# Performance work log

Hardware: AMD Instinct MI355X
Metric: run time of the kernel (lower is better)

Reference implementation:

```python
import jax, jax.numpy as jnp
import numpy as np

B, N, M, K = 128, 20000, 85400, 3  # trajectories, variables, clauses, literals/clause


def setup_inputs() -> dict:
    key = jax.random.key(0)
    k_v, k_idx, k_sign, k_xs = jax.random.split(key, 4)
    v = jax.random.normal(k_v, (B, N), dtype=jnp.float32)
    input_idx = jax.random.randint(k_idx, (B, M, K), 0, N, dtype=jnp.int32)
    # literal signs are exactly +/-1
    input_sign = jnp.where(jax.random.normal(k_sign, (B, M, K)) > 0, 1.0, -1.0).astype(jnp.float32)
    xl = jnp.ones((B, M), dtype=jnp.float32)            # long-term memory (init 1)
    xs = jax.random.uniform(k_xs, (B, M), dtype=jnp.float32)  # short-term memory in [0,1]
    # [alpha, beta, gamma, delta, epsilon, zeta] -- typical MemComputing coefficients
    param = jnp.array([5.0, 20.0, 0.25, 0.05, 0.001, 0.1], dtype=jnp.float32)
    return {"v": v, "xl": xl, "xs": xs, "param": param,
            "input_sign": input_sign, "input_idx": input_idx}


def reference(v, xl, xs, param, input_sign, input_idx):
    """Faithful port of OR.calc_grad. Returns (C, grad_v, dxl, dxs)."""
    b = v.shape[0]
    k = input_idx.shape[-1]
    alpha, beta, gamma, delta, epsilon, zeta = param
    b_idx = jnp.arange(b)[:, None, None]                # (B,1,1)
    inp = v[b_idx, input_idx] * input_sign              # (B,M,K) gather + sign
    v_top, v_top_idx = jax.lax.top_k(inp, 2)            # top-2 literal values per clause
    v_top = (1.0 - v_top) * 0.5                         # transform; v_top[...,0] is smallest -> C
    C = v_top[..., 0]                                   # (B,M) clause 'distance to satisfied'
    hot = jax.nn.one_hot(v_top_idx[..., 0], k, dtype=v.dtype)  # (B,M,K) mask of max literal
    # G: C everywhere, second-best value at the max-literal slot, scaled by xl*xs
    G = jnp.where(hot > 0, v_top[..., 1:2], C[..., None]) * (xl * xs)[..., None]
    # R: C only at the max-literal slot, scaled by (1+zeta*xl)*(1-xs)
    R = hot * C[..., None] * ((1.0 + zeta * xl) * (1.0 - xs))[..., None]
    dv = -(G + R) * input_sign                          # (B,M,K)
    grad_v = jnp.zeros_like(v).at[b_idx, input_idx].add(dv)  # scatter-add over dim 1
    dxl = -alpha * (C - delta)                          # (B,M)
    dxs = -beta * (xs + epsilon) * (C - gamma)          # (B,M)
    return C, grad_v, dxl, dxs
```

## Files before the change

### kernel.cpp

```cpp
#include <hip/hip_runtime.h>


#define NMAX 20000
#define BPB  4

typedef int   int4v   __attribute__((ext_vector_type(4)));
typedef float float4v __attribute__((ext_vector_type(4)));

__device__ __forceinline__ void clause_math(
    float a0, float a1, float a2, float xlv, float xsv, float zeta,
    float& C, float& g0, float& g1, float& g2)
{
    int k0; float m0, m1;
    if (a0 >= a1) {
        if (a0 >= a2) { k0 = 0; m0 = a0; m1 = fmaxf(a1, a2); }
        else          { k0 = 2; m0 = a2; m1 = fmaxf(a0, a1); }
    } else {
        if (a1 >= a2) { k0 = 1; m0 = a1; m1 = fmaxf(a0, a2); }
        else          { k0 = 2; m0 = a2; m1 = fmaxf(a0, a1); }
    }
    C = (1.f - m0) * 0.5f;
    const float T2 = (1.f - m1) * 0.5f;
    const float gl = xlv * xsv;
    const float rC = C * ((1.f + zeta * xlv) * (1.f - xsv));
    g0 = (k0 == 0 ? T2 : C) * gl + (k0 == 0 ? rC : 0.f);
    g1 = (k0 == 1 ? T2 : C) * gl + (k0 == 1 ? rC : 0.f);
    g2 = (k0 == 2 ? T2 : C) * gl + (k0 == 2 ? rC : 0.f);
}

__global__ __launch_bounds__(1024, 1) void or_priv2(
    const float* __restrict__ v,
    const float* __restrict__ xl,
    const float* __restrict__ xs,
    const float* __restrict__ param,
    const float* __restrict__ sign,
    const int*   __restrict__ idx,
    float* __restrict__ outC,
    float* __restrict__ outdxl,
    float* __restrict__ outdxs,
    float* __restrict__ partial,
    int N, int M, int chunk)
{
    __shared__ float sv[NMAX];
    __shared__ float sg[NMAX];
    const int j = blockIdx.x;
    const int b = blockIdx.y;
    const int tid = threadIdx.x;

    {
        const float4v* __restrict__ v4 = (const float4v*)(v + (size_t)b * N);
        float4v* sv4 = (float4v*)sv;
        float4v* sg4 = (float4v*)sg;
        const int n4 = N >> 2;
        const float4v z = {0.f, 0.f, 0.f, 0.f};
        for (int i = tid; i < n4; i += 1024) {
            sv4[i] = v4[i];
            sg4[i] = z;
        }
        for (int i = (n4 << 2) + tid; i < N; i += 1024) {
            sv[i] = v[(size_t)b * N + i];
            sg[i] = 0.f;
        }
    }
    __syncthreads();

    const float alpha = param[0], beta = param[1], gamma = param[2];
    const float delta = param[3], eps  = param[4], zeta  = param[5];

    const int mstart = j * chunk;
    const int mend   = min(M, mstart + chunk);
    const int ngroups = (mend > mstart) ? ((mend - mstart + 3) >> 2) : 0;

    for (int g = tid; g < ngroups; g += 1024) {
        const int m0 = mstart + (g << 2);
        const size_t base = (size_t)b * M + m0;

        if (m0 + 3 < mend) {
            const int4v*   __restrict__ ip = (const int4v*)(idx + base * 3);
            const float4v* __restrict__ sp = (const float4v*)(sign + base * 3);
            const int4v   ia = __builtin_nontemporal_load(ip + 0);
            const int4v   ib = __builtin_nontemporal_load(ip + 1);
            const int4v   ic = __builtin_nontemporal_load(ip + 2);
            const float4v sa = __builtin_nontemporal_load(sp + 0);
            const float4v sb = __builtin_nontemporal_load(sp + 1);
            const float4v sc = __builtin_nontemporal_load(sp + 2);
            const float4v xl4 = __builtin_nontemporal_load((const float4v*)(xl + base));
            const float4v xs4 = __builtin_nontemporal_load((const float4v*)(xs + base));

            const int   ii[12] = {ia.x, ia.y, ia.z, ia.w, ib.x, ib.y, ib.z, ib.w,
                                  ic.x, ic.y, ic.z, ic.w};
            const float ss[12] = {sa.x, sa.y, sa.z, sa.w, sb.x, sb.y, sb.z, sb.w,
                                  sc.x, sc.y, sc.z, sc.w};
            const float xlA[4] = {xl4.x, xl4.y, xl4.z, xl4.w};
            const float xsA[4] = {xs4.x, xs4.y, xs4.z, xs4.w};
            float Cv[4], dxlv[4], dxsv[4];

            #pragma unroll
            for (int c = 0; c < 4; ++c) {
                const int   i0 = ii[3*c], i1 = ii[3*c+1], i2 = ii[3*c+2];
                const float s0 = ss[3*c], s1 = ss[3*c+1], s2 = ss[3*c+2];
                const float a0 = sv[i0] * s0, a1 = sv[i1] * s1, a2 = sv[i2] * s2;
                float C, g0, g1, g2;
                clause_math(a0, a1, a2, xlA[c], xsA[c], zeta, C, g0, g1, g2);
                atomicAdd(&sg[i0], -g0 * s0);
                atomicAdd(&sg[i1], -g1 * s1);
                atomicAdd(&sg[i2], -g2 * s2);
                Cv[c]   = C;
                dxlv[c] = -alpha * (C - delta);
                dxsv[c] = -beta * (xsA[c] + eps) * (C - gamma);
            }
            const float4v cv  = {Cv[0], Cv[1], Cv[2], Cv[3]};
            const float4v lv  = {dxlv[0], dxlv[1], dxlv[2], dxlv[3]};
            const float4v svo = {dxsv[0], dxsv[1], dxsv[2], dxsv[3]};
            __builtin_nontemporal_store(cv,  (float4v*)(outC + base));
            __builtin_nontemporal_store(lv,  (float4v*)(outdxl + base));
            __builtin_nontemporal_store(svo, (float4v*)(outdxs + base));
        } else {
            for (int m = m0; m < mend; ++m) {
                const size_t bm  = (size_t)b * M + m;
                const size_t bm3 = bm * 3;
                const int   i0 = idx[bm3 + 0], i1 = idx[bm3 + 1], i2 = idx[bm3 + 2];
                const float s0 = sign[bm3 + 0], s1 = sign[bm3 + 1], s2 = sign[bm3 + 2];
                const float a0 = sv[i0] * s0, a1 = sv[i1] * s1, a2 = sv[i2] * s2;
                const float xlv = xl[bm], xsv = xs[bm];
                float C, g0, g1, g2;
                clause_math(a0, a1, a2, xlv, xsv, zeta, C, g0, g1, g2);
                atomicAdd(&sg[i0], -g0 * s0);
                atomicAdd(&sg[i1], -g1 * s1);
                atomicAdd(&sg[i2], -g2 * s2);
                outC[bm]   = C;
                outdxl[bm] = -alpha * (C - delta);
                outdxs[bm] = -beta * (xsv + eps) * (C - gamma);
            }
        }
    }
    __syncthreads();

    {
        float* __restrict__ pj = partial + ((size_t)j * gridDim.y + b) * N;
        const float4v* sg4 = (const float4v*)sg;
        const int n4 = N >> 2;
        for (int i = tid; i < n4; i += 1024)
            __builtin_nontemporal_store(sg4[i], (float4v*)pj + i);
        for (int i = (n4 << 2) + tid; i < N; i += 1024) pj[i] = sg[i];
    }
}

__global__ __launch_bounds__(256) void reduce4(
    const float4v* __restrict__ p, float4v* __restrict__ out, int n4, int stride4)
{
    int i = blockIdx.x * 256 + threadIdx.x;
    const int gs = gridDim.x * 256;
    for (; i < n4; i += gs) {
        const float4v a = p[i];
        const float4v b = p[i + stride4];
        const float4v c = p[i + 2 * stride4];
        const float4v d = p[i + 3 * stride4];
        out[i] = a + b + c + d;
    }
}

__global__ __launch_bounds__(256) void zero_f4(float4v* __restrict__ p, int n4) {
    int i = blockIdx.x * blockDim.x + threadIdx.x;
    int stride = gridDim.x * blockDim.x;
    const float4v z = {0.f, 0.f, 0.f, 0.f};
    for (; i < n4; i += stride) p[i] = z;
}

__global__ __launch_bounds__(256) void or_kernel(
    const float* __restrict__ v, const float* __restrict__ xl,
    const float* __restrict__ xs, const float* __restrict__ param,
    const float* __restrict__ sign, const int* __restrict__ idx,
    float* __restrict__ outC, float* __restrict__ gradv,
    float* __restrict__ outdxl, float* __restrict__ outdxs, int N, int M)
{
    const int m = blockIdx.x * blockDim.x + threadIdx.x;
    const int b = blockIdx.y;
    if (m >= M) return;
    const size_t bm = (size_t)b * M + m;
    const size_t bm3 = bm * 3;
    const int   i0 = idx[bm3 + 0], i1 = idx[bm3 + 1], i2 = idx[bm3 + 2];
    const float s0 = sign[bm3 + 0], s1 = sign[bm3 + 1], s2 = sign[bm3 + 2];
    const float* __restrict__ vb = v + (size_t)b * N;
    const float a0 = vb[i0] * s0, a1 = vb[i1] * s1, a2 = vb[i2] * s2;
    const float xlv = xl[bm], xsv = xs[bm];
    const float alpha = param[0], beta = param[1], gamma = param[2];
    const float delta = param[3], eps  = param[4], zeta  = param[5];

    float C, g0, g1, g2;
    clause_math(a0, a1, a2, xlv, xsv, zeta, C, g0, g1, g2);

    float* __restrict__ gb = gradv + (size_t)b * N;
    atomicAdd(&gb[i0], -g0 * s0);
    atomicAdd(&gb[i1], -g1 * s1);
    atomicAdd(&gb[i2], -g2 * s2);

    outC[bm]   = C;
    outdxl[bm] = -alpha * (C - delta);
    outdxs[bm] = -beta * (xsv + eps) * (C - gamma);
}

extern "C" void kernel_launch(void* const* d_in, const int* in_sizes, int n_in,
                              void* d_out, int out_size, void* d_ws, size_t ws_size,
                              hipStream_t stream) {
    const float* v     = (const float*)d_in[0];
    const float* xl    = (const float*)d_in[1];
    const float* xs    = (const float*)d_in[2];
    const float* param = (const float*)d_in[3];
    const float* sign  = (const float*)d_in[4];
    const int*   idx   = (const int*)d_in[5];

    const int B = 128;
    const int N = in_sizes[0] / B;
    const int M = in_sizes[1] / B;

    float* outC   = (float*)d_out;
    float* gradv  = outC   + (size_t)in_sizes[1];
    float* outdxl = gradv  + (size_t)in_sizes[0];
    float* outdxs = outdxl + (size_t)in_sizes[1];

    const size_t bn = (size_t)B * N;
    const size_t ws_need = (size_t)BPB * bn * sizeof(float);

    if (N <= NMAX && ws_size >= ws_need && (bn % 4) == 0 && (M % 4) == 0) {
        float* partial = (float*)d_ws;
        const int chunk = (((M + BPB - 1) / BPB) + 3) & ~3;
        dim3 grid(BPB, B);
        or_priv2<<<grid, dim3(1024), 0, stream>>>(v, xl, xs, param, sign, idx,
                                                  outC, outdxl, outdxs, partial,
                                                  N, M, chunk);
        const int n4 = (int)(bn / 4);
        const int rblocks = min(2048, (n4 + 255) / 256);
        reduce4<<<dim3(rblocks), dim3(256), 0, stream>>>(
            (const float4v*)partial, (float4v*)gradv, n4, n4);
    } else {
        const int n4 = (int)(bn / 4);
        zero_f4<<<dim3((n4 + 255) / 256), dim3(256), 0, stream>>>((float4v*)gradv, n4);
        dim3 grid((M + 255) / 256, B);
        or_kernel<<<grid, dim3(256), 0, stream>>>(v, xl, xs, param, sign, idx,
                                                  outC, gradv, outdxl, outdxs, N, M);
    }
}
```

Baseline: 473.2 us.

## Gather v from global through L2 and remap blocks so each XCD shares trajectories

Drops the shared-memory copy of v, which halves LDS use per block (80KB to 40KB) and lets two 1024-thread blocks fit per CU. The v gathers now go to global memory and rely on L2. Block IDs are remapped so that the four chunk-blocks of one trajectory land on the same XCD under round-robin dispatch, which is meant to improve L2 reuse of v. The LDS atomics switch to unsafeAtomicAdd, which should emit native ds_add_f32 instead of CAS loops. The risk is higher latency on the scattered global gathers compared with LDS reads.

```diff
diff --git a/kernel.cpp b/kernel.cpp
--- a/kernel.cpp
+++ b/kernel.cpp
@@ -28,7 +28,7 @@
     g2 = (k0 == 2 ? T2 : C) * gl + (k0 == 2 ? rC : 0.f);
 }
 
-__global__ __launch_bounds__(1024, 1) void or_priv2(
+__global__ __launch_bounds__(1024, 8) void or_priv3(
     const float* __restrict__ v,
     const float* __restrict__ xl,
     const float* __restrict__ xs,
@@ -39,33 +39,30 @@
     float* __restrict__ outdxl,
     float* __restrict__ outdxs,
     float* __restrict__ partial,
-    int N, int M, int chunk)
-{
-    __shared__ float sv[NMAX];
+    int N, int M, int B, int chunk)
+{
     __shared__ float sg[NMAX];
-    const int j = blockIdx.x;
-    const int b = blockIdx.y;
+
+    const int id  = blockIdx.x;
+    const int cpx = gridDim.x >> 3;
+    const int cid = (id & 7) * cpx + (id >> 3);
+    const int b   = cid >> 2;
+    const int j   = cid & 3;
     const int tid = threadIdx.x;
 
     {
-        const float4v* __restrict__ v4 = (const float4v*)(v + (size_t)b * N);
-        float4v* sv4 = (float4v*)sv;
         float4v* sg4 = (float4v*)sg;
+        const float4v z = {0.f, 0.f, 0.f, 0.f};
         const int n4 = N >> 2;
-        const float4v z = {0.f, 0.f, 0.f, 0.f};
-        for (int i = tid; i < n4; i += 1024) {
-            sv4[i] = v4[i];
-            sg4[i] = z;
-        }
-        for (int i = (n4 << 2) + tid; i < N; i += 1024) {
-            sv[i] = v[(size_t)b * N + i];
-            sg[i] = 0.f;
-        }
+        for (int i = tid; i < n4; i += 1024) sg4[i] = z;
+        for (int i = (n4 << 2) + tid; i < N; i += 1024) sg[i] = 0.f;
     }
     __syncthreads();
 
     const float alpha = param[0], beta = param[1], gamma = param[2];
     const float delta = param[3], eps  = param[4], zeta  = param[5];
+
+    const float* __restrict__ vb = v + (size_t)b * N;
 
     const int mstart = j * chunk;
     const int mend   = min(M, mstart + chunk);
@@ -99,12 +96,12 @@
             for (int c = 0; c < 4; ++c) {
                 const int   i0 = ii[3*c], i1 = ii[3*c+1], i2 = ii[3*c+2];
                 const float s0 = ss[3*c], s1 = ss[3*c+1], s2 = ss[3*c+2];
-                const float a0 = sv[i0] * s0, a1 = sv[i1] * s1, a2 = sv[i2] * s2;
+                const float a0 = vb[i0] * s0, a1 = vb[i1] * s1, a2 = vb[i2] * s2;
                 float C, g0, g1, g2;
                 clause_math(a0, a1, a2, xlA[c], xsA[c], zeta, C, g0, g1, g2);
-                atomicAdd(&sg[i0], -g0 * s0);
-                atomicAdd(&sg[i1], -g1 * s1);
-                atomicAdd(&sg[i2], -g2 * s2);
+                unsafeAtomicAdd(&sg[i0], -g0 * s0);
+                unsafeAtomicAdd(&sg[i1], -g1 * s1);
+                unsafeAtomicAdd(&sg[i2], -g2 * s2);
                 Cv[c]   = C;
                 dxlv[c] = -alpha * (C - delta);
                 dxsv[c] = -beta * (xsA[c] + eps) * (C - gamma);
@@ -121,13 +118,13 @@
                 const size_t bm3 = bm * 3;
                 const int   i0 = idx[bm3 + 0], i1 = idx[bm3 + 1], i2 = idx[bm3 + 2];
                 const float s0 = sign[bm3 + 0], s1 = sign[bm3 + 1], s2 = sign[bm3 + 2];
-                const float a0 = sv[i0] * s0, a1 = sv[i1] * s1, a2 = sv[i2] * s2;
+                const float a0 = vb[i0] * s0, a1 = vb[i1] * s1, a2 = vb[i2] * s2;
                 const float xlv = xl[bm], xsv = xs[bm];
                 float C, g0, g1, g2;
                 clause_math(a0, a1, a2, xlv, xsv, zeta, C, g0, g1, g2);
-                atomicAdd(&sg[i0], -g0 * s0);
-                atomicAdd(&sg[i1], -g1 * s1);
-                atomicAdd(&sg[i2], -g2 * s2);
+                unsafeAtomicAdd(&sg[i0], -g0 * s0);
+                unsafeAtomicAdd(&sg[i1], -g1 * s1);
+                unsafeAtomicAdd(&sg[i2], -g2 * s2);
                 outC[bm]   = C;
                 outdxl[bm] = -alpha * (C - delta);
                 outdxs[bm] = -beta * (xsv + eps) * (C - gamma);
@@ -137,7 +134,7 @@
     __syncthreads();
 
     {
-        float* __restrict__ pj = partial + ((size_t)j * gridDim.y + b) * N;
+        float* __restrict__ pj = partial + ((size_t)j * B + b) * N;
         const float4v* sg4 = (const float4v*)sg;
         const int n4 = N >> 2;
         for (int i = tid; i < n4; i += 1024)
@@ -225,10 +222,9 @@
     if (N <= NMAX && ws_size >= ws_need && (bn % 4) == 0 && (M % 4) == 0) {
         float* partial = (float*)d_ws;
         const int chunk = (((M + BPB - 1) / BPB) + 3) & ~3;
-        dim3 grid(BPB, B);
-        or_priv2<<<grid, dim3(1024), 0, stream>>>(v, xl, xs, param, sign, idx,
-                                                  outC, outdxl, outdxs, partial,
-                                                  N, M, chunk);
+        or_priv3<<<dim3(BPB * B), dim3(1024), 0, stream>>>(
+            v, xl, xs, param, sign, idx, outC, outdxl, outdxs,
+            (float*)partial, N, M, B, chunk);
         const int n4 = (int)(bn / 4);
         const int rblocks = min(2048, (n4 + 255) / 256);
         reduce4<<<dim3(rblocks), dim3(256), 0, stream>>>(
```

Result: slower. 511.2 us (+8.0%).
